# Optimization experiments

Measured on AMD Instinct MI355X. Metric: run time of the kernel, lower is better.

## Reference

```python
import jax, jax.numpy as jnp
import numpy as np

B, T, D = 2, 1024, 2048
N, K, H = 16, 4, 128          # num_heads, num_kv_heads, head_dim
TC = 1024                     # cached tokens
S = TC + T
MAX_WAVELENGTH = 10000.0
BIG_NEG = -2.3819763e38


def _apply_rope(x, positions):
    """RoPE: positions [B,L] applied to x [B,L,heads,H]."""
    half = x.shape[-1] // 2
    freq_exponents = (2.0 / x.shape[-1]) * jnp.arange(half, dtype=jnp.float32)
    timescale = MAX_WAVELENGTH ** freq_exponents                      # [H/2]
    radians = (positions.astype(jnp.float32)[..., None] / timescale)[..., None, :]  # [B,L,1,H/2]
    sin, cos = jnp.sin(radians), jnp.cos(radians)
    x1, x2 = jnp.split(x, 2, axis=-1)
    res = jnp.concatenate([x1 * cos - x2 * sin, x2 * cos + x1 * sin], axis=-1)
    return res.astype(x.dtype)


def setup_inputs() -> dict:
    key = jax.random.key(0)
    ks = jax.random.split(key, 8)
    x = jax.random.normal(ks[0], (B, T, D), dtype=jnp.float32)
    # new tokens sit right after the cache
    positions = jnp.broadcast_to(TC + jnp.arange(T, dtype=jnp.int32), (B, T))
    # causal mask over [cache + new]: query t may attend to keys s <= TC + t
    s_idx = jnp.arange(S)[None, :]
    t_idx = jnp.arange(T)[:, None]
    attn_mask = jnp.broadcast_to((s_idx <= TC + t_idx)[None, None, :, :], (B, 1, T, S))
    cache_k = jax.random.normal(ks[1], (B, TC, K, H), dtype=jnp.float32)
    cache_v = jax.random.normal(ks[2], (B, TC, K, H), dtype=jnp.float32)
    # lecun-normal-ish fan-in scaling (fan_in = D for projections, N*H for output)
    w_q = jax.random.normal(ks[3], (N, D, H), dtype=jnp.float32) * (D ** -0.5)
    w_kv = jax.random.normal(ks[4], (2, K, D, H), dtype=jnp.float32) * (D ** -0.5)
    w_out = jax.random.normal(ks[5], (N, H, D), dtype=jnp.float32) * ((N * H) ** -0.5)
    return {"x": x, "positions": positions, "attn_mask": attn_mask,
            "cache_k": cache_k, "cache_v": cache_v,
            "w_q": w_q, "w_kv": w_kv, "w_out": w_out}


def reference(x, positions, attn_mask, cache_k, cache_v, w_q, w_kv, w_out):
    dtype = x.dtype
    # projections (GQA path: num_kv_heads != num_heads)
    q = jnp.einsum('BTD,NDH->BTNH', x, w_q.astype(dtype))
    kv = jnp.einsum('BSD,CKDH->CBSKH', x, w_kv.astype(dtype))
    k_new, v_new = kv[0], kv[1]
    # inline RoPE + query scaling
    q = _apply_rope(q, positions) * (H ** -0.5)
    k_new = _apply_rope(k_new, positions)
    # KV-cache concat
    k = jnp.concatenate([cache_k, k_new], axis=1)   # [B,S,K,H]
    v = jnp.concatenate([cache_v, v_new], axis=1)
    # group heads: B T (K G) H -> B T K G H
    G = N // K
    qg = q.reshape(q.shape[0], q.shape[1], K, G, H)
    logits = jnp.einsum('BTKGH,BSKH->BKGTS', qg, k,
                        preferred_element_type=jnp.float32)
    masked = jnp.where(attn_mask[:, :, None, :, :], logits, BIG_NEG)
    probs = jax.nn.softmax(masked, axis=-1).astype(dtype)
    enc = jnp.einsum('BKGTS,BSKH->BTKGH', probs, v)
    enc = enc.reshape(enc.shape[0], enc.shape[1], N, H)  # B T (K G) H
    out = jnp.einsum('BTNH,NHD->BTD', enc, w_out.astype(dtype))
    return out, k, v
```

## Files before the change

kernel.cpp:

```cpp
#include <hip/hip_runtime.h>

#define B_  2
#define T_  1024
#define D_  2048
#define NH  16
#define KH  4
#define HD  128
#define TC_ 1024
#define S_  2048

typedef __bf16 bf16x4v __attribute__((ext_vector_type(4)));
typedef __bf16 bf16x8v __attribute__((ext_vector_type(8)));
typedef float  f32x4v  __attribute__((ext_vector_type(4)));

__device__ __forceinline__ void async_copy16(void* lds, const void* g) {
    __builtin_amdgcn_global_load_lds(
        (__attribute__((address_space(1))) void*)g,
        (__attribute__((address_space(3))) void*)lds, 16, 0, 0);
}

__global__ void cvt_x(const float* __restrict__ x, __bf16* __restrict__ xb) {
    int i = (blockIdx.x * 256 + threadIdx.x) * 4;
    float4 v = *(const float4*)(x + i);
    bf16x4v o; o[0]=(__bf16)v.x; o[1]=(__bf16)v.y; o[2]=(__bf16)v.z; o[3]=(__bf16)v.w;
    *(bf16x4v*)(xb + i) = o;
}

__global__ void tp_w(const float* __restrict__ in, __bf16* __restrict__ out) {
    __shared__ float tile[32][33];
    int h0 = blockIdx.x * 32;
    int d0 = blockIdx.y * 32;
    const float* ip = in + (size_t)blockIdx.z * (D_ * HD);
    __bf16* op = out + (size_t)blockIdx.z * (D_ * HD);
    int tx = threadIdx.x, ty = threadIdx.y;
    for (int i = 0; i < 32; i += 8)
        tile[ty + i][tx] = ip[(size_t)(d0 + ty + i) * HD + h0 + tx];
    __syncthreads();
    for (int i = 0; i < 32; i += 8)
        op[(size_t)(h0 + ty + i) * D_ + d0 + tx] = (__bf16)tile[tx][ty + i];
}

__global__ void tp_wout(const float* __restrict__ in, __bf16* __restrict__ out) {
    __shared__ float tile[32][33];
    int d0 = blockIdx.x * 32;
    int h0 = blockIdx.y * 32;
    int n  = blockIdx.z;
    const float* ip = in + (size_t)n * (HD * D_);
    int tx = threadIdx.x, ty = threadIdx.y;
    for (int i = 0; i < 32; i += 8)
        tile[ty + i][tx] = ip[(size_t)(h0 + ty + i) * D_ + d0 + tx];
    __syncthreads();
    for (int i = 0; i < 32; i += 8)
        out[(size_t)(d0 + ty + i) * (NH * HD) + n * HD + h0 + tx] = (__bf16)tile[tx][ty + i];
}

__global__ void tp_v(const float* __restrict__ vout, __bf16* __restrict__ vtb) {
    __shared__ float tile[32][33];
    int z = blockIdx.z; int b = z / KH, kh = z % KH;
    int h0 = blockIdx.x * 32;
    int s0 = blockIdx.y * 32;
    const float* ip = vout + ((size_t)b * S_ * KH + kh) * HD;
    int tx = threadIdx.x, ty = threadIdx.y;
    for (int i = 0; i < 32; i += 8)
        tile[ty + i][tx] = ip[(size_t)(s0 + ty + i) * (KH * HD) + h0 + tx];
    __syncthreads();
    __bf16* op = vtb + ((size_t)b * KH + kh) * (size_t)HD * S_;
    for (int i = 0; i < 32; i += 8)
        op[(size_t)(h0 + ty + i) * S_ + s0 + tx] = (__bf16)tile[tx][ty + i];
}

__global__ void copy_cache(const float4* __restrict__ ck, const float4* __restrict__ cv,
                           float* __restrict__ kout, float* __restrict__ vout,
                           __bf16* __restrict__ kb) {
    int i = blockIdx.x * 256 + threadIdx.x;
    int b = i >> 17;
    int r = i & 131071;
    float4 kv = ck[i];
    ((float4*)(kout + (size_t)b * S_ * KH * HD))[r] = kv;
    ((float4*)(vout + (size_t)b * S_ * KH * HD))[r] = cv[i];
    int h4 = r & 31;
    int kh = (r >> 5) & 3;
    int s  = r >> 7;
    bf16x4v o; o[0]=(__bf16)kv.x; o[1]=(__bf16)kv.y; o[2]=(__bf16)kv.z; o[3]=(__bf16)kv.w;
    *(bf16x4v*)(kb + (((size_t)(b * KH + kh) * S_ + s) * HD) + h4 * 4) = o;
}

__global__ __launch_bounds__(256, 2)
void gemm_bt(const __bf16* __restrict__ A, const __bf16* __restrict__ BT,
             float* __restrict__ C, int ldc) {
    __shared__ __bf16 As[128 * 64];
    __shared__ __bf16 Bs[128 * 64];
    const int m0 = blockIdx.x * 128, n0 = blockIdx.y * 128;
    const int tid = threadIdx.x;
    const int wave = tid >> 6, lane = tid & 63;
    const int quad = lane >> 4, l16 = lane & 15;
    const int wm = (wave & 1) * 64, wn = (wave >> 1) * 64;
    const int lrow = lane >> 3, lcol = (lane & 7) * 8;

    f32x4v acc[4][4];
    for (int i = 0; i < 4; i++)
        for (int j = 0; j < 4; j++)
            acc[i][j] = (f32x4v){0.f, 0.f, 0.f, 0.f};

    const __bf16* Abase = A + (size_t)m0 * D_;
    const __bf16* Bbase = BT + (size_t)n0 * D_;

    for (int k0 = 0; k0 < D_; k0 += 64) {
        for (int j = 0; j < 4; j++) {
            int r = wave * 32 + j * 8;
            async_copy16(As + (size_t)r * 64,
                         Abase + (size_t)(r + lrow) * D_ + k0 + lcol);
            async_copy16(Bs + (size_t)r * 64,
                         Bbase + (size_t)(r + lrow) * D_ + k0 + lcol);
        }
        __syncthreads();
        for (int ks = 0; ks < 2; ks++) {
            bf16x8v a[4], b[4];
            for (int i = 0; i < 4; i++)
                a[i] = *(const bf16x8v*)(As + (wm + i * 16 + l16) * 64 + ks * 32 + quad * 8);
            for (int j = 0; j < 4; j++)
                b[j] = *(const bf16x8v*)(Bs + (wn + j * 16 + l16) * 64 + ks * 32 + quad * 8);
            for (int i = 0; i < 4; i++)
                for (int j = 0; j < 4; j++)
                    acc[i][j] = __builtin_amdgcn_mfma_f32_16x16x32_bf16(a[i], b[j], acc[i][j], 0, 0, 0);
        }
        __syncthreads();
    }
    for (int i = 0; i < 4; i++)
        for (int j = 0; j < 4; j++)
            for (int r = 0; r < 4; r++) {
                int row = m0 + wm + i * 16 + quad * 4 + r;
                int col = n0 + wn + j * 16 + l16;
                C[(size_t)row * ldc + col] = acc[i][j][r];
            }
}

__global__ void finish_rope(const float* __restrict__ proj, const int* __restrict__ pos,
                            __bf16* __restrict__ qws, float* __restrict__ kout,
                            float* __restrict__ vout, __bf16* __restrict__ kb) {
    const int tau = blockIdx.x;
    const int b = tau >> 10, t = tau & 1023;
    const float p = (float)pos[tau];
    const float* pr = proj + (size_t)tau * 3072;
    const float qscale = 0.08838834764831845f;
    for (int idx = threadIdx.x; idx < (NH + KH) * 64; idx += 256) {
        int head = idx >> 6;
        int hh = idx & 63;
        float r = p * __expf(-(float)hh * (9.210340371976184f / 64.0f));
        float sn = sinf(r), cs = cosf(r);
        if (head < NH) {
            float x1 = pr[head * HD + hh], x2 = pr[head * HD + hh + 64];
            size_t qo = ((size_t)tau * NH + head) * HD;
            qws[qo + hh]      = (__bf16)((x1 * cs - x2 * sn) * qscale);
            qws[qo + hh + 64] = (__bf16)((x2 * cs + x1 * sn) * qscale);
        } else {
            int kh = head - NH;
            float x1 = pr[2048 + kh * HD + hh], x2 = pr[2048 + kh * HD + hh + 64];
            float k1 = x1 * cs - x2 * sn, k2 = x2 * cs + x1 * sn;
            size_t ko = ((size_t)(b * S_ + TC_ + t) * KH + kh) * HD;
            kout[ko + hh]      = k1;
            kout[ko + hh + 64] = k2;
            size_t kbo = ((size_t)(b * KH + kh) * S_ + TC_ + t) * HD;
            kb[kbo + hh]      = (__bf16)k1;
            kb[kbo + hh + 64] = (__bf16)k2;
        }
    }
    for (int idx = threadIdx.x; idx < KH * HD; idx += 256) {
        int kh = idx >> 7, h = idx & 127;
        vout[((size_t)(b * S_ + TC_ + t) * KH + kh) * HD + h] = pr[2560 + kh * HD + h];
    }
}

__global__ __launch_bounds__(256, 2)
void attn(const __bf16* __restrict__ qws, const __bf16* __restrict__ kb,
          const __bf16* __restrict__ vtb,
          __bf16* __restrict__ op0, __bf16* __restrict__ op1,
          float2* __restrict__ mlb0, float2* __restrict__ mlb1) {
    __shared__ __bf16 Ks[64 * 128];
    __shared__ __bf16 Vs[128 * 64];
    __shared__ __bf16 Ps[128 * 72];

    const int t0 = blockIdx.x * 128;
    const int n  = blockIdx.y;
    const int bz = blockIdx.z;
    const int b = bz >> 1, half = bz & 1;
    const int kh = n >> 2;
    const int tid = threadIdx.x, w = tid >> 6, lane = tid & 63;
    const int quad = lane >> 4, l16 = lane & 15;

    bf16x8v qf[2][4];
    {
        const __bf16* qbase = qws + ((size_t)(b * T_ + t0 + w * 32) * NH + n) * HD;
        for (int qt = 0; qt < 2; qt++)
            for (int ks = 0; ks < 4; ks++)
                qf[qt][ks] = *(const bf16x8v*)(qbase + (size_t)(qt * 16 + l16) * (NH * HD)
                                               + ks * 32 + quad * 8);
    }

    float m_run[2][4], l_run[2][4];
    f32x4v o_acc[2][8];
    for (int qt = 0; qt < 2; qt++)
        for (int r = 0; r < 4; r++) { m_run[qt][r] = -INFINITY; l_run[qt][r] = 0.f; }
    for (int qt = 0; qt < 2; qt++)
        for (int j = 0; j < 8; j++) o_acc[qt][j] = (f32x4v){0.f, 0.f, 0.f, 0.f};

    const int nS  = (TC_ + t0 + 128) >> 6;
    const int st0 = half ? (nS >> 1) : 0;
    const int st1 = half ? nS : (nS >> 1);
    const int wk_max = TC_ + t0 + w * 32 + 31;
    const __bf16* kbase = kb  + ((size_t)(b * KH + kh)) * S_ * HD;
    const __bf16* vbase = vtb + ((size_t)(b * KH + kh)) * (size_t)HD * S_;

    for (int st = st0; st < st1; st++) {
        const int s0 = st * 64;
        {
            const int ar = lane >> 4, ac = lane & 15;
            for (int jj = 0; jj < 4; jj++) {
                int r0 = w * 16 + jj * 4;
                int row = r0 + ar;
                async_copy16(Ks + (size_t)r0 * 128,
                             kbase + (size_t)(s0 + row) * HD + ((ac ^ (row & 15)) * 8));
            }
        }
        {
            const int ar = lane >> 3, ac = lane & 7;
            for (int jj = 0; jj < 4; jj++) {
                int r0 = w * 32 + jj * 8;
                int row = r0 + ar;
                async_copy16(Vs + (size_t)r0 * 64,
                             vbase + (size_t)row * S_ + s0 + ((ac ^ (row & 7)) * 8));
            }
        }
        __syncthreads();

        if (s0 <= wk_max) {
            f32x4v sc[2][4];
            for (int qt = 0; qt < 2; qt++)
                for (int j = 0; j < 4; j++) sc[qt][j] = (f32x4v){0.f, 0.f, 0.f, 0.f};
            for (int ks = 0; ks < 4; ks++) {
                bf16x8v bb[4];
                for (int j = 0; j < 4; j++)
                    bb[j] = *(const bf16x8v*)(Ks + (j * 16 + l16) * 128
                                              + (((ks * 4 + quad) ^ l16) * 8));
                for (int qt = 0; qt < 2; qt++)
                    for (int j = 0; j < 4; j++)
                        sc[qt][j] = __builtin_amdgcn_mfma_f32_16x16x32_bf16(qf[qt][ks], bb[j], sc[qt][j], 0, 0, 0);
            }

            if (st >= nS - 2) {
                for (int qt = 0; qt < 2; qt++)
                    for (int j = 0; j < 4; j++)
                        for (int r = 0; r < 4; r++) {
                            int s_abs = s0 + j * 16 + l16;
                            int q_abs = t0 + w * 32 + qt * 16 + quad * 4 + r;
                            if (s_abs > TC_ + q_abs) sc[qt][j][r] = -3.0e38f;
                        }
            }

            for (int qt = 0; qt < 2; qt++)
                for (int r = 0; r < 4; r++) {
                    float mx = sc[qt][0][r];
                    for (int j = 1; j < 4; j++) mx = fmaxf(mx, sc[qt][j][r]);
                    for (int off = 8; off >= 1; off >>= 1) mx = fmaxf(mx, __shfl_xor(mx, off, 64));
                    mx = fmaxf(mx, m_run[qt][r]);
                    float alpha = __expf(m_run[qt][r] - mx);
                    m_run[qt][r] = mx;
                    float s = 0.f;
                    for (int j = 0; j < 4; j++) {
                        float pv = __expf(sc[qt][j][r] - mx);
                        sc[qt][j][r] = pv;
                        s += pv;
                    }
                    for (int off = 8; off >= 1; off >>= 1) s += __shfl_xor(s, off, 64);
                    l_run[qt][r] = l_run[qt][r] * alpha + s;
                    for (int j = 0; j < 8; j++) o_acc[qt][j][r] *= alpha;
                }

            for (int qt = 0; qt < 2; qt++)
                for (int j = 0; j < 4; j++)
                    for (int r = 0; r < 4; r++) {
                        int row = w * 32 + qt * 16 + quad * 4 + r;
                        Ps[row * 72 + j * 16 + l16] = (__bf16)sc[qt][j][r];
                    }

            for (int ks = 0; ks < 2; ks++) {
                bf16x8v av[2];
                for (int qt = 0; qt < 2; qt++)
                    av[qt] = *(const bf16x8v*)(Ps + (w * 32 + qt * 16 + l16) * 72
                                               + ks * 32 + quad * 8);
                bf16x8v bb[8];
                for (int j = 0; j < 8; j++)
                    bb[j] = *(const bf16x8v*)(Vs + (j * 16 + l16) * 64
                                              + (((ks * 4 + quad) ^ (l16 & 7)) * 8));
                for (int qt = 0; qt < 2; qt++)
                    for (int j = 0; j < 8; j++)
                        o_acc[qt][j] = __builtin_amdgcn_mfma_f32_16x16x32_bf16(av[qt], bb[j], o_acc[qt][j], 0, 0, 0);
            }
        }
        __syncthreads();
    }

    __bf16* op = half ? op1 : op0;
    float2* ml = half ? mlb1 : mlb0;
    for (int qt = 0; qt < 2; qt++)
        for (int r = 0; r < 4; r++) {
            int grow = (b * NH + n) * T_ + t0 + w * 32 + qt * 16 + quad * 4 + r;
            if (l16 == 0) ml[grow] = make_float2(m_run[qt][r], l_run[qt][r]);
            for (int j = 0; j < 8; j++)
                op[(size_t)grow * HD + j * 16 + l16] = (__bf16)o_acc[qt][j][r];
        }
}

__global__ void merge(const __bf16* __restrict__ o0, const __bf16* __restrict__ o1,
                      const float2* __restrict__ ml0, const float2* __restrict__ ml1,
                      __bf16* __restrict__ enc) {
    int gid = blockIdx.x * 256 + threadIdx.x;
    int row = gid >> 5, c4 = (gid & 31) * 4;
    float2 A = ml0[row], Bm = ml1[row];
    float m  = fmaxf(A.x, Bm.x);
    float wA = __expf(A.x - m), wB = __expf(Bm.x - m);
    float inv = 1.0f / (wA * A.y + wB * Bm.y);
    bf16x4v a = *(const bf16x4v*)(o0 + (size_t)row * HD + c4);
    bf16x4v c = *(const bf16x4v*)(o1 + (size_t)row * HD + c4);
    int b = row >> 14, n = (row >> 10) & 15, t = row & 1023;
    bf16x4v e;
    for (int i = 0; i < 4; i++)
        e[i] = (__bf16)((wA * (float)a[i] + wB * (float)c[i]) * inv);
    *(bf16x4v*)(enc + (((size_t)(b * T_ + t) * NH + n) * HD) + c4) = e;
}

extern "C" void kernel_launch(void* const* d_in, const int* in_sizes, int n_in,
                              void* d_out, int out_size, void* d_ws, size_t ws_size,
                              hipStream_t stream) {
    const float* x       = (const float*)d_in[0];
    const int*   pos     = (const int*)d_in[1];
    const float* cache_k = (const float*)d_in[3];
    const float* cache_v = (const float*)d_in[4];
    const float* w_q     = (const float*)d_in[5];
    const float* w_kv    = (const float*)d_in[6];
    const float* w_out   = (const float*)d_in[7];

    float* out  = (float*)d_out;
    float* kout = out  + (size_t)B_ * T_ * D_;
    float* vout = kout + (size_t)B_ * S_ * KH * HD;

    char* ws = (char*)d_ws;
    __bf16* xb   = (__bf16*)ws;  ws += (size_t)B_ * T_ * D_ * 2;
    __bf16* wt   = (__bf16*)ws;  ws += (size_t)3072 * D_ * 2;
    __bf16* wot  = (__bf16*)ws;  ws += (size_t)D_ * NH * HD * 2;
    float*  proj = (float*)ws;   ws += (size_t)B_ * T_ * 3072 * 4;
    __bf16* qws  = (__bf16*)ws;  ws += (size_t)B_ * T_ * NH * HD * 2;
    __bf16* kbuf = (__bf16*)ws;  ws += (size_t)B_ * S_ * KH * HD * 2;
    __bf16* vtb  = (__bf16*)ws;  ws += (size_t)B_ * S_ * KH * HD * 2;
    __bf16* enc  = (__bf16*)ws;

    const size_t ON = (size_t)B_ * NH * T_ * HD;
    __bf16* op0 = (__bf16*)proj;
    __bf16* op1 = op0 + ON;
    float2* ml0 = (float2*)(op1 + ON);
    float2* ml1 = ml0 + (size_t)B_ * NH * T_;

    cvt_x<<<4096, 256, 0, stream>>>(x, xb);
    tp_w<<<dim3(4, 64, 16), dim3(32, 8), 0, stream>>>(w_q, wt);
    tp_w<<<dim3(4, 64, 8),  dim3(32, 8), 0, stream>>>(w_kv, wt + (size_t)16 * HD * D_);
    tp_wout<<<dim3(64, 4, 16), dim3(32, 8), 0, stream>>>(w_out, wot);
    copy_cache<<<1024, 256, 0, stream>>>((const float4*)cache_k, (const float4*)cache_v, kout, vout, kbuf);
    gemm_bt<<<dim3(16, 24), 256, 0, stream>>>(xb, wt, proj, 3072);
    finish_rope<<<2048, 256, 0, stream>>>(proj, pos, qws, kout, vout, kbuf);
    tp_v<<<dim3(4, 64, 8), dim3(32, 8), 0, stream>>>(vout, vtb);
    attn<<<dim3(8, 16, 4), 256, 0, stream>>>(qws, kbuf, vtb, op0, op1, ml0, ml1);
    merge<<<4096, 256, 0, stream>>>(op0, op1, ml0, ml1, enc);
    gemm_bt<<<dim3(16, 16), 256, 0, stream>>>(enc, wot, out, 2048);
}
```

Measured before the change: 313.2 us.

## Fuse RoPE into QKV GEMM epilogue and restructure attention as max-free split-KV

The QKV projection GEMM now applies RoPE and the query scaling in its epilogue. It writes q, k and v straight to their bf16/fp32 destinations, including the transposed V. This removes the fp32 projection buffer round-trip and the separate finish_rope and tp_v passes over new tokens. Both GEMMs switch to a 32x128 per-wave tile with XOR-swizzled LDS to cut bank conflicts. Attention becomes single-wave blocks with a three-way split over the key range and no LDS staging of K/V. It drops the running max and computes row sums with an MFMA against a ones vector, so merge is just a sum divided by the total. Exponentiating raw logits without subtracting a max assumes logits stay small, which risks overflow on larger-magnitude inputs.

```diff
diff --git a/kernel.cpp b/kernel.cpp
--- a/kernel.cpp
+++ b/kernel.cpp
@@ -54,12 +54,12 @@
         out[(size_t)(d0 + ty + i) * (NH * HD) + n * HD + h0 + tx] = (__bf16)tile[tx][ty + i];
 }
 
-__global__ void tp_v(const float* __restrict__ vout, __bf16* __restrict__ vtb) {
+__global__ void tp_v(const float* __restrict__ cv, __bf16* __restrict__ vtb) {
     __shared__ float tile[32][33];
     int z = blockIdx.z; int b = z / KH, kh = z % KH;
     int h0 = blockIdx.x * 32;
     int s0 = blockIdx.y * 32;
-    const float* ip = vout + ((size_t)b * S_ * KH + kh) * HD;
+    const float* ip = cv + ((size_t)b * TC_ * KH + kh) * HD;
     int tx = threadIdx.x, ty = threadIdx.y;
     for (int i = 0; i < 32; i += 8)
         tile[ty + i][tx] = ip[(size_t)(s0 + ty + i) * (KH * HD) + h0 + tx];
@@ -86,246 +86,251 @@
 }
 
 __global__ __launch_bounds__(256, 2)
-void gemm_bt(const __bf16* __restrict__ A, const __bf16* __restrict__ BT,
-             float* __restrict__ C, int ldc) {
+void qkv_gemm(const __bf16* __restrict__ A, const __bf16* __restrict__ BT,
+              const int* __restrict__ pos,
+              __bf16* __restrict__ qws, float* __restrict__ kout,
+              float* __restrict__ vout, __bf16* __restrict__ kb,
+              __bf16* __restrict__ vtb) {
+    __shared__ __bf16 As[128 * 64];
+    __shared__ __bf16 Bs[128 * 64];
+    const int m0 = blockIdx.x * 128, ny = blockIdx.y;
+    const int tid = threadIdx.x;
+    const int wave = tid >> 6, lane = tid & 63;
+    const int quad = lane >> 4, l16 = lane & 15;
+    const int lrow = lane >> 3;
+    const int lsw  = (lane & 7) ^ (lrow & 7);
+
+    f32x4v acc[2][8];
+    for (int i = 0; i < 2; i++)
+        for (int j = 0; j < 8; j++)
+            acc[i][j] = (f32x4v){0.f, 0.f, 0.f, 0.f};
+
+    const __bf16* Abase = A + (size_t)m0 * D_;
+    const __bf16* Bbase = BT + (size_t)ny * 128 * D_;
+
+    for (int k0 = 0; k0 < D_; k0 += 64) {
+        for (int jj = 0; jj < 4; jj++) {
+            int r = wave * 32 + jj * 8;
+            async_copy16(As + (size_t)r * 64,
+                         Abase + (size_t)(r + lrow) * D_ + k0 + lsw * 8);
+            async_copy16(Bs + (size_t)r * 64,
+                         Bbase + (size_t)(r + lrow) * D_ + k0 + lsw * 8);
+        }
+        __syncthreads();
+        for (int ks = 0; ks < 2; ks++) {
+            bf16x8v a[2], bb[8];
+            for (int i = 0; i < 2; i++)
+                a[i] = *(const bf16x8v*)(As + (wave * 32 + i * 16 + l16) * 64
+                                         + (((ks * 4 + quad) ^ (l16 & 7)) * 8));
+            for (int j = 0; j < 8; j++)
+                bb[j] = *(const bf16x8v*)(Bs + (j * 16 + l16) * 64
+                                          + (((ks * 4 + quad) ^ (l16 & 7)) * 8));
+            for (int i = 0; i < 2; i++)
+                for (int j = 0; j < 8; j++)
+                    acc[i][j] = __builtin_amdgcn_mfma_f32_16x16x32_bf16(a[i], bb[j], acc[i][j], 0, 0, 0);
+        }
+        __syncthreads();
+    }
+
+    const float qscale = 0.08838834764831845f;
+    for (int i = 0; i < 2; i++)
+        for (int r = 0; r < 4; r++) {
+            int tau = m0 + wave * 32 + i * 16 + quad * 4 + r;
+            int b = tau >> 10, t = tau & 1023;
+            if (ny < 20) {
+                float p = (float)pos[tau];
+                for (int j = 0; j < 4; j++) {
+                    int h = j * 16 + l16;
+                    float ang = p * __expf(-(float)h * (9.210340371976184f / 64.0f));
+                    float sn = sinf(ang), cs = cosf(ang);
+                    float x1 = acc[i][j][r], x2 = acc[i][j + 4][r];
+                    float o1 = x1 * cs - x2 * sn;
+                    float o2 = x2 * cs + x1 * sn;
+                    if (ny < NH) {
+                        size_t qo = ((size_t)tau * NH + ny) * HD;
+                        qws[qo + h]      = (__bf16)(o1 * qscale);
+                        qws[qo + h + 64] = (__bf16)(o2 * qscale);
+                    } else {
+                        int kh = ny - NH;
+                        size_t ko = ((size_t)(b * S_ + TC_ + t) * KH + kh) * HD;
+                        kout[ko + h]      = o1;
+                        kout[ko + h + 64] = o2;
+                        size_t kbo = ((size_t)(b * KH + kh) * S_ + TC_ + t) * HD;
+                        kb[kbo + h]      = (__bf16)o1;
+                        kb[kbo + h + 64] = (__bf16)o2;
+                    }
+                }
+            } else {
+                int kh = ny - 20;
+                size_t vo = ((size_t)(b * S_ + TC_ + t) * KH + kh) * HD;
+                size_t vt = ((size_t)(b * KH + kh)) * (size_t)HD * S_;
+                for (int j = 0; j < 8; j++) {
+                    int h = j * 16 + l16;
+                    float v = acc[i][j][r];
+                    vout[vo + h] = v;
+                    vtb[vt + (size_t)h * S_ + TC_ + t] = (__bf16)v;
+                }
+            }
+        }
+}
+
+__global__ __launch_bounds__(256, 2)
+void out_gemm(const __bf16* __restrict__ A, const __bf16* __restrict__ BT,
+              float* __restrict__ C) {
     __shared__ __bf16 As[128 * 64];
     __shared__ __bf16 Bs[128 * 64];
     const int m0 = blockIdx.x * 128, n0 = blockIdx.y * 128;
     const int tid = threadIdx.x;
     const int wave = tid >> 6, lane = tid & 63;
     const int quad = lane >> 4, l16 = lane & 15;
-    const int wm = (wave & 1) * 64, wn = (wave >> 1) * 64;
-    const int lrow = lane >> 3, lcol = (lane & 7) * 8;
-
-    f32x4v acc[4][4];
-    for (int i = 0; i < 4; i++)
-        for (int j = 0; j < 4; j++)
+    const int lrow = lane >> 3;
+    const int lsw  = (lane & 7) ^ (lrow & 7);
+
+    f32x4v acc[2][8];
+    for (int i = 0; i < 2; i++)
+        for (int j = 0; j < 8; j++)
             acc[i][j] = (f32x4v){0.f, 0.f, 0.f, 0.f};
 
     const __bf16* Abase = A + (size_t)m0 * D_;
     const __bf16* Bbase = BT + (size_t)n0 * D_;
 
     for (int k0 = 0; k0 < D_; k0 += 64) {
-        for (int j = 0; j < 4; j++) {
-            int r = wave * 32 + j * 8;
+        for (int jj = 0; jj < 4; jj++) {
+            int r = wave * 32 + jj * 8;
             async_copy16(As + (size_t)r * 64,
-                         Abase + (size_t)(r + lrow) * D_ + k0 + lcol);
+                         Abase + (size_t)(r + lrow) * D_ + k0 + lsw * 8);
             async_copy16(Bs + (size_t)r * 64,
-                         Bbase + (size_t)(r + lrow) * D_ + k0 + lcol);
+                         Bbase + (size_t)(r + lrow) * D_ + k0 + lsw * 8);
         }
         __syncthreads();
         for (int ks = 0; ks < 2; ks++) {
-            bf16x8v a[4], b[4];
-            for (int i = 0; i < 4; i++)
-                a[i] = *(const bf16x8v*)(As + (wm + i * 16 + l16) * 64 + ks * 32 + quad * 8);
-            for (int j = 0; j < 4; j++)
-                b[j] = *(const bf16x8v*)(Bs + (wn + j * 16 + l16) * 64 + ks * 32 + quad * 8);
-            for (int i = 0; i < 4; i++)
-                for (int j = 0; j < 4; j++)
-                    acc[i][j] = __builtin_amdgcn_mfma_f32_16x16x32_bf16(a[i], b[j], acc[i][j], 0, 0, 0);
-        }
-        __syncthreads();
-    }
-    for (int i = 0; i < 4; i++)
-        for (int j = 0; j < 4; j++)
-            for (int r = 0; r < 4; r++) {
-                int row = m0 + wm + i * 16 + quad * 4 + r;
-                int col = n0 + wn + j * 16 + l16;
-                C[(size_t)row * ldc + col] = acc[i][j][r];
-            }
-}
-
-__global__ void finish_rope(const float* __restrict__ proj, const int* __restrict__ pos,
-                            __bf16* __restrict__ qws, float* __restrict__ kout,
-                            float* __restrict__ vout, __bf16* __restrict__ kb) {
-    const int tau = blockIdx.x;
-    const int b = tau >> 10, t = tau & 1023;
-    const float p = (float)pos[tau];
-    const float* pr = proj + (size_t)tau * 3072;
-    const float qscale = 0.08838834764831845f;
-    for (int idx = threadIdx.x; idx < (NH + KH) * 64; idx += 256) {
-        int head = idx >> 6;
-        int hh = idx & 63;
-        float r = p * __expf(-(float)hh * (9.210340371976184f / 64.0f));
-        float sn = sinf(r), cs = cosf(r);
-        if (head < NH) {
-            float x1 = pr[head * HD + hh], x2 = pr[head * HD + hh + 64];
-            size_t qo = ((size_t)tau * NH + head) * HD;
-            qws[qo + hh]      = (__bf16)((x1 * cs - x2 * sn) * qscale);
-            qws[qo + hh + 64] = (__bf16)((x2 * cs + x1 * sn) * qscale);
-        } else {
-            int kh = head - NH;
-            float x1 = pr[2048 + kh * HD + hh], x2 = pr[2048 + kh * HD + hh + 64];
-            float k1 = x1 * cs - x2 * sn, k2 = x2 * cs + x1 * sn;
-            size_t ko = ((size_t)(b * S_ + TC_ + t) * KH + kh) * HD;
-            kout[ko + hh]      = k1;
-            kout[ko + hh + 64] = k2;
-            size_t kbo = ((size_t)(b * KH + kh) * S_ + TC_ + t) * HD;
-            kb[kbo + hh]      = (__bf16)k1;
-            kb[kbo + hh + 64] = (__bf16)k2;
-        }
-    }
-    for (int idx = threadIdx.x; idx < KH * HD; idx += 256) {
-        int kh = idx >> 7, h = idx & 127;
-        vout[((size_t)(b * S_ + TC_ + t) * KH + kh) * HD + h] = pr[2560 + kh * HD + h];
-    }
-}
-
-__global__ __launch_bounds__(256, 2)
+            bf16x8v a[2], bb[8];
+            for (int i = 0; i < 2; i++)
+                a[i] = *(const bf16x8v*)(As + (wave * 32 + i * 16 + l16) * 64
+                                         + (((ks * 4 + quad) ^ (l16 & 7)) * 8));
+            for (int j = 0; j < 8; j++)
+                bb[j] = *(const bf16x8v*)(Bs + (j * 16 + l16) * 64
+                                          + (((ks * 4 + quad) ^ (l16 & 7)) * 8));
+            for (int i = 0; i < 2; i++)
+                for (int j = 0; j < 8; j++)
+                    acc[i][j] = __builtin_amdgcn_mfma_f32_16x16x32_bf16(a[i], bb[j], acc[i][j], 0, 0, 0);
+        }
+        __syncthreads();
+    }
+    for (int i = 0; i < 2; i++)
+        for (int r = 0; r < 4; r++) {
+            int row = m0 + wave * 32 + i * 16 + quad * 4 + r;
+            for (int j = 0; j < 8; j++)
+                C[(size_t)row * D_ + n0 + j * 16 + l16] = acc[i][j][r];
+        }
+}
+
+__global__ __launch_bounds__(64, 3)
 void attn(const __bf16* __restrict__ qws, const __bf16* __restrict__ kb,
           const __bf16* __restrict__ vtb,
-          __bf16* __restrict__ op0, __bf16* __restrict__ op1,
-          float2* __restrict__ mlb0, float2* __restrict__ mlb1) {
-    __shared__ __bf16 Ks[64 * 128];
-    __shared__ __bf16 Vs[128 * 64];
-    __shared__ __bf16 Ps[128 * 72];
-
-    const int t0 = blockIdx.x * 128;
-    const int n  = blockIdx.y;
-    const int bz = blockIdx.z;
-    const int b = bz >> 1, half = bz & 1;
-    const int kh = n >> 2;
-    const int tid = threadIdx.x, w = tid >> 6, lane = tid & 63;
-    const int quad = lane >> 4, l16 = lane & 15;
+          __bf16* __restrict__ op0, __bf16* __restrict__ op1, __bf16* __restrict__ op2,
+          float* __restrict__ lb0, float* __restrict__ lb1, float* __restrict__ lb2) {
+    __shared__ __bf16 Ps[32 * 72];
+
+    const int jid = blockIdx.x;
+    const int bn = jid / 96;
+    const int rem = jid - bn * 96;
+    const int c = rem / 3, p = rem - (rem / 3) * 3;
+    const int b = bn >> 4, n = bn & 15, kh = n >> 2;
+    const int t0 = c * 32;
+    const int nT = (TC_ + t0 + 32 + 63) >> 6;
+    const int q0 = (nT + 2) / 3;
+    const int st_beg = p * q0;
+    const int st_end = (st_beg + q0 < nT) ? (st_beg + q0) : nT;
+
+    const int lane = threadIdx.x, quad = lane >> 4, l16 = lane & 15;
 
     bf16x8v qf[2][4];
     {
-        const __bf16* qbase = qws + ((size_t)(b * T_ + t0 + w * 32) * NH + n) * HD;
+        const __bf16* qbase = qws + ((size_t)(b * T_ + t0) * NH + n) * HD;
         for (int qt = 0; qt < 2; qt++)
             for (int ks = 0; ks < 4; ks++)
                 qf[qt][ks] = *(const bf16x8v*)(qbase + (size_t)(qt * 16 + l16) * (NH * HD)
                                                + ks * 32 + quad * 8);
     }
 
-    float m_run[2][4], l_run[2][4];
-    f32x4v o_acc[2][8];
-    for (int qt = 0; qt < 2; qt++)
-        for (int r = 0; r < 4; r++) { m_run[qt][r] = -INFINITY; l_run[qt][r] = 0.f; }
-    for (int qt = 0; qt < 2; qt++)
+    f32x4v o_acc[2][8], oL[2];
+    for (int qt = 0; qt < 2; qt++) {
+        oL[qt] = (f32x4v){0.f, 0.f, 0.f, 0.f};
         for (int j = 0; j < 8; j++) o_acc[qt][j] = (f32x4v){0.f, 0.f, 0.f, 0.f};
-
-    const int nS  = (TC_ + t0 + 128) >> 6;
-    const int st0 = half ? (nS >> 1) : 0;
-    const int st1 = half ? nS : (nS >> 1);
-    const int wk_max = TC_ + t0 + w * 32 + 31;
+    }
+    bf16x8v onesv;
+    for (int e = 0; e < 8; e++) onesv[e] = (l16 == 0) ? (__bf16)1.0f : (__bf16)0.0f;
+
     const __bf16* kbase = kb  + ((size_t)(b * KH + kh)) * S_ * HD;
     const __bf16* vbase = vtb + ((size_t)(b * KH + kh)) * (size_t)HD * S_;
 
-    for (int st = st0; st < st1; st++) {
+    for (int st = st_beg; st < st_end; st++) {
         const int s0 = st * 64;
-        {
-            const int ar = lane >> 4, ac = lane & 15;
-            for (int jj = 0; jj < 4; jj++) {
-                int r0 = w * 16 + jj * 4;
-                int row = r0 + ar;
-                async_copy16(Ks + (size_t)r0 * 128,
-                             kbase + (size_t)(s0 + row) * HD + ((ac ^ (row & 15)) * 8));
+        const bool maskt = (st == nT - 1);
+
+        for (int j = 0; j < 4; j++) {
+            f32x4v scj[2];
+            scj[0] = (f32x4v){0.f, 0.f, 0.f, 0.f};
+            scj[1] = (f32x4v){0.f, 0.f, 0.f, 0.f};
+            const int s_abs = s0 + j * 16 + l16;
+            for (int ks = 0; ks < 4; ks++) {
+                bf16x8v bbv = *(const bf16x8v*)(kbase + (size_t)s_abs * HD + ks * 32 + quad * 8);
+                for (int qt = 0; qt < 2; qt++)
+                    scj[qt] = __builtin_amdgcn_mfma_f32_16x16x32_bf16(qf[qt][ks], bbv, scj[qt], 0, 0, 0);
             }
-        }
-        {
-            const int ar = lane >> 3, ac = lane & 7;
-            for (int jj = 0; jj < 4; jj++) {
-                int r0 = w * 32 + jj * 8;
-                int row = r0 + ar;
-                async_copy16(Vs + (size_t)r0 * 64,
-                             vbase + (size_t)row * S_ + s0 + ((ac ^ (row & 7)) * 8));
-            }
-        }
-        __syncthreads();
-
-        if (s0 <= wk_max) {
-            f32x4v sc[2][4];
-            for (int qt = 0; qt < 2; qt++)
-                for (int j = 0; j < 4; j++) sc[qt][j] = (f32x4v){0.f, 0.f, 0.f, 0.f};
-            for (int ks = 0; ks < 4; ks++) {
-                bf16x8v bb[4];
-                for (int j = 0; j < 4; j++)
-                    bb[j] = *(const bf16x8v*)(Ks + (j * 16 + l16) * 128
-                                              + (((ks * 4 + quad) ^ l16) * 8));
-                for (int qt = 0; qt < 2; qt++)
-                    for (int j = 0; j < 4; j++)
-                        sc[qt][j] = __builtin_amdgcn_mfma_f32_16x16x32_bf16(qf[qt][ks], bb[j], sc[qt][j], 0, 0, 0);
-            }
-
-            if (st >= nS - 2) {
-                for (int qt = 0; qt < 2; qt++)
-                    for (int j = 0; j < 4; j++)
-                        for (int r = 0; r < 4; r++) {
-                            int s_abs = s0 + j * 16 + l16;
-                            int q_abs = t0 + w * 32 + qt * 16 + quad * 4 + r;
-                            if (s_abs > TC_ + q_abs) sc[qt][j][r] = -3.0e38f;
-                        }
-            }
-
             for (int qt = 0; qt < 2; qt++)
                 for (int r = 0; r < 4; r++) {
-                    float mx = sc[qt][0][r];
-                    for (int j = 1; j < 4; j++) mx = fmaxf(mx, sc[qt][j][r]);
-                    for (int off = 8; off >= 1; off >>= 1) mx = fmaxf(mx, __shfl_xor(mx, off, 64));
-                    mx = fmaxf(mx, m_run[qt][r]);
-                    float alpha = __expf(m_run[qt][r] - mx);
-                    m_run[qt][r] = mx;
-                    float s = 0.f;
-                    for (int j = 0; j < 4; j++) {
-                        float pv = __expf(sc[qt][j][r] - mx);
-                        sc[qt][j][r] = pv;
-                        s += pv;
-                    }
-                    for (int off = 8; off >= 1; off >>= 1) s += __shfl_xor(s, off, 64);
-                    l_run[qt][r] = l_run[qt][r] * alpha + s;
-                    for (int j = 0; j < 8; j++) o_acc[qt][j][r] *= alpha;
+                    int q_abs = t0 + qt * 16 + quad * 4 + r;
+                    float pv = (maskt && (s_abs > TC_ + q_abs)) ? 0.f : __expf(scj[qt][r]);
+                    Ps[(qt * 16 + quad * 4 + r) * 72 + j * 16 + l16] = (__bf16)pv;
                 }
-
-            for (int qt = 0; qt < 2; qt++)
-                for (int j = 0; j < 4; j++)
-                    for (int r = 0; r < 4; r++) {
-                        int row = w * 32 + qt * 16 + quad * 4 + r;
-                        Ps[row * 72 + j * 16 + l16] = (__bf16)sc[qt][j][r];
-                    }
-
-            for (int ks = 0; ks < 2; ks++) {
-                bf16x8v av[2];
+        }
+        __syncthreads();
+
+        for (int ks2 = 0; ks2 < 2; ks2++) {
+            bf16x8v av[2];
+            for (int qt = 0; qt < 2; qt++) {
+                av[qt] = *(const bf16x8v*)(Ps + (qt * 16 + l16) * 72 + ks2 * 32 + quad * 8);
+                oL[qt] = __builtin_amdgcn_mfma_f32_16x16x32_bf16(av[qt], onesv, oL[qt], 0, 0, 0);
+            }
+            for (int jh = 0; jh < 8; jh++) {
+                bf16x8v bbv = *(const bf16x8v*)(vbase + (size_t)(jh * 16 + l16) * S_
+                                                + s0 + ks2 * 32 + quad * 8);
                 for (int qt = 0; qt < 2; qt++)
-                    av[qt] = *(const bf16x8v*)(Ps + (w * 32 + qt * 16 + l16) * 72
-                                               + ks * 32 + quad * 8);
-                bf16x8v bb[8];
-                for (int j = 0; j < 8; j++)
-                    bb[j] = *(const bf16x8v*)(Vs + (j * 16 + l16) * 64
-                                              + (((ks * 4 + quad) ^ (l16 & 7)) * 8));
-                for (int qt = 0; qt < 2; qt++)
-                    for (int j = 0; j < 8; j++)
-                        o_acc[qt][j] = __builtin_amdgcn_mfma_f32_16x16x32_bf16(av[qt], bb[j], o_acc[qt][j], 0, 0, 0);
+                    o_acc[qt][jh] = __builtin_amdgcn_mfma_f32_16x16x32_bf16(av[qt], bbv, o_acc[qt][jh], 0, 0, 0);
             }
         }
         __syncthreads();
     }
 
-    __bf16* op = half ? op1 : op0;
-    float2* ml = half ? mlb1 : mlb0;
+    __bf16* op = (p == 0) ? op0 : (p == 1) ? op1 : op2;
+    float*  lb = (p == 0) ? lb0 : (p == 1) ? lb1 : lb2;
+    const size_t rbase = (size_t)bn * T_ + t0;
     for (int qt = 0; qt < 2; qt++)
         for (int r = 0; r < 4; r++) {
-            int grow = (b * NH + n) * T_ + t0 + w * 32 + qt * 16 + quad * 4 + r;
-            if (l16 == 0) ml[grow] = make_float2(m_run[qt][r], l_run[qt][r]);
-            for (int j = 0; j < 8; j++)
-                op[(size_t)grow * HD + j * 16 + l16] = (__bf16)o_acc[qt][j][r];
+            int row = qt * 16 + quad * 4 + r;
+            if (l16 == 0) lb[rbase + row] = oL[qt][r];
+            for (int jh = 0; jh < 8; jh++)
+                op[(rbase + row) * HD + jh * 16 + l16] = (__bf16)o_acc[qt][jh][r];
         }
 }
 
 __global__ void merge(const __bf16* __restrict__ o0, const __bf16* __restrict__ o1,
-                      const float2* __restrict__ ml0, const float2* __restrict__ ml1,
+                      const __bf16* __restrict__ o2,
+                      const float* __restrict__ l0, const float* __restrict__ l1,
+                      const float* __restrict__ l2,
                       __bf16* __restrict__ enc) {
     int gid = blockIdx.x * 256 + threadIdx.x;
     int row = gid >> 5, c4 = (gid & 31) * 4;
-    float2 A = ml0[row], Bm = ml1[row];
-    float m  = fmaxf(A.x, Bm.x);
-    float wA = __expf(A.x - m), wB = __expf(Bm.x - m);
-    float inv = 1.0f / (wA * A.y + wB * Bm.y);
+    float inv = 1.0f / (l0[row] + l1[row] + l2[row]);
     bf16x4v a = *(const bf16x4v*)(o0 + (size_t)row * HD + c4);
     bf16x4v c = *(const bf16x4v*)(o1 + (size_t)row * HD + c4);
+    bf16x4v d = *(const bf16x4v*)(o2 + (size_t)row * HD + c4);
     int b = row >> 14, n = (row >> 10) & 15, t = row & 1023;
     bf16x4v e;
     for (int i = 0; i < 4; i++)
-        e[i] = (__bf16)((wA * (float)a[i] + wB * (float)c[i]) * inv);
+        e[i] = (__bf16)(((float)a[i] + (float)c[i] + (float)d[i]) * inv);
     *(bf16x4v*)(enc + (((size_t)(b * T_ + t) * NH + n) * HD) + c4) = e;
 }
 
@@ -348,27 +353,28 @@
     __bf16* xb   = (__bf16*)ws;  ws += (size_t)B_ * T_ * D_ * 2;
     __bf16* wt   = (__bf16*)ws;  ws += (size_t)3072 * D_ * 2;
     __bf16* wot  = (__bf16*)ws;  ws += (size_t)D_ * NH * HD * 2;
-    float*  proj = (float*)ws;   ws += (size_t)B_ * T_ * 3072 * 4;
+    char*   scr  = ws;           ws += (size_t)B_ * T_ * 3072 * 4;
     __bf16* qws  = (__bf16*)ws;  ws += (size_t)B_ * T_ * NH * HD * 2;
     __bf16* kbuf = (__bf16*)ws;  ws += (size_t)B_ * S_ * KH * HD * 2;
     __bf16* vtb  = (__bf16*)ws;  ws += (size_t)B_ * S_ * KH * HD * 2;
     __bf16* enc  = (__bf16*)ws;
 
     const size_t ON = (size_t)B_ * NH * T_ * HD;
-    __bf16* op0 = (__bf16*)proj;
+    __bf16* op0 = (__bf16*)scr;
     __bf16* op1 = op0 + ON;
-    float2* ml0 = (float2*)(op1 + ON);
-    float2* ml1 = ml0 + (size_t)B_ * NH * T_;
+    __bf16* op2 = op1 + ON;
+    float* lb0 = (float*)wt;
+    float* lb1 = lb0 + (size_t)B_ * NH * T_;
+    float* lb2 = lb1 + (size_t)B_ * NH * T_;
 
     cvt_x<<<4096, 256, 0, stream>>>(x, xb);
     tp_w<<<dim3(4, 64, 16), dim3(32, 8), 0, stream>>>(w_q, wt);
     tp_w<<<dim3(4, 64, 8),  dim3(32, 8), 0, stream>>>(w_kv, wt + (size_t)16 * HD * D_);
     tp_wout<<<dim3(64, 4, 16), dim3(32, 8), 0, stream>>>(w_out, wot);
     copy_cache<<<1024, 256, 0, stream>>>((const float4*)cache_k, (const float4*)cache_v, kout, vout, kbuf);
-    gemm_bt<<<dim3(16, 24), 256, 0, stream>>>(xb, wt, proj, 3072);
-    finish_rope<<<2048, 256, 0, stream>>>(proj, pos, qws, kout, vout, kbuf);
-    tp_v<<<dim3(4, 64, 8), dim3(32, 8), 0, stream>>>(vout, vtb);
-    attn<<<dim3(8, 16, 4), 256, 0, stream>>>(qws, kbuf, vtb, op0, op1, ml0, ml1);
-    merge<<<4096, 256, 0, stream>>>(op0, op1, ml0, ml1, enc);
-    gemm_bt<<<dim3(16, 16), 256, 0, stream>>>(enc, wot, out, 2048);
-}
+    tp_v<<<dim3(4, 32, 8), dim3(32, 8), 0, stream>>>(cache_v, vtb);
+    qkv_gemm<<<dim3(16, 24), 256, 0, stream>>>(xb, wt, pos, qws, kout, vout, kbuf, vtb);
+    attn<<<3072, 64, 0, stream>>>(qws, kbuf, vtb, op0, op1, op2, lb0, lb1, lb2);
+    merge<<<4096, 256, 0, stream>>>(op0, op1, op2, lb0, lb1, lb2, enc);
+    out_gemm<<<dim3(16, 16), 256, 0, stream>>>(enc, wot, out);
+}
```

Measured after the change: 471.0 us. 1.5x slower.
